# Kernel tuning notes

Measured on AMD Instinct MI355X. Metric: run time of the kernel, lower is better.

## Reference

```python
import jax, jax.numpy as jnp
import numpy as np

B, S, H, TOK = 64, 512, 768, 8   # batch rows, tokens/row, hidden, tokens per sentence
K = (B * S) // TOK               # 4096 sentence segments
NUM_CLASSES = 4


def setup_inputs() -> dict:
    key = jax.random.key(0)
    k0, k1, k2, k3 = jax.random.split(key, 4)
    out = jax.random.normal(k0, (B, S, H), dtype=jnp.float32)
    # each row i holds sentences i*64 .. i*64+63, 8 contiguous tokens each
    sent_ids = (jnp.arange(B * S, dtype=jnp.int64) // TOK).reshape(B, S)
    labels = jax.random.randint(k1, (B, S), 0, NUM_CLASSES, dtype=jnp.int64)
    W1 = jax.random.normal(k2, (2 * H, 512), dtype=jnp.float32) * 0.02
    b1 = jnp.zeros((512,), dtype=jnp.float32)
    W2 = jax.random.normal(k3, (512, NUM_CLASSES), dtype=jnp.float32) * 0.02
    b2 = jnp.zeros((NUM_CLASSES,), dtype=jnp.float32)
    return {"out": out, "W1": W1, "b1": b1, "W2": W2, "b2": b2,
            "labels": labels, "sent_ids": sent_ids}


def _ner_forward(out, W1, b1, W2, b2, labels, sent_ids):
    ids = sent_ids.reshape(-1)                      # [B*S]
    x = out.reshape(-1, H)                          # [B*S, H]
    n = ids.shape[0]
    valid = ids >= 0                                # -1 means padding
    seg = jnp.where(valid, ids, K).astype(jnp.int32)  # route invalid to dummy slot K
    w = valid.astype(out.dtype)

    # masked segment mean of token embeddings (avg_vector)
    counts = jax.ops.segment_sum(w, seg, num_segments=K + 1)[:K]            # [K]
    sums = jax.ops.segment_sum(x * w[:, None], seg, num_segments=K + 1)[:K]  # [K,H]
    seg_mean = sums / jnp.maximum(counts, 1.0)[:, None]

    # build_dict: cls vector of segment k = out[i][0] of LAST row containing k
    row = jnp.arange(n) // S
    cls_row = jax.ops.segment_max(jnp.where(valid, row, -1), seg, num_segments=K + 1)[:K]
    cls_vec = out[jnp.maximum(cls_row, 0), 0]       # [K, H]

    # segment label = labels[mask][0] (first token in flattened order)
    first_idx = jax.ops.segment_min(jnp.where(valid, jnp.arange(n), n), seg,
                                    num_segments=K + 1)[:K]
    seg_label = labels.reshape(-1)[jnp.minimum(first_idx, n - 1)]  # [K]

    feats = jnp.concatenate([cls_vec, seg_mean], axis=1)  # [K, 2H]
    h = jax.nn.relu(feats @ W1 + b1)                      # dropout is identity in eval
    probs = jax.nn.softmax(h @ W2 + b2, axis=1)           # [K, 4]

    # Multiclass_Focal_Loss: gather prob at label, -log, sorted truncated sum
    p = jnp.take_along_axis(probs, seg_label[:, None].astype(jnp.int32), axis=1)[:, 0]
    costs = -jnp.log(p)                                   # [K]
    pos = seg_label > 0
    Npos = jnp.sum(pos)
    neg_costs = jnp.where(seg_label == 0, costs, -jnp.inf)
    sorted_desc = -jnp.sort(-neg_costs)                   # descending
    M = jnp.floor(2.5 * Npos.astype(jnp.float32)).astype(jnp.int32)
    take = (jnp.arange(K) < M) & jnp.isfinite(sorted_desc)
    total = jnp.sum(jnp.where(pos, costs, 0.0)) + jnp.sum(jnp.where(take, sorted_desc, 0.0))
    denom = jnp.floor(3.5 * Npos.astype(jnp.float32))
    return total / denom


def reference(out, W1, b1, W2, b2, labels, sent_ids):
    return _ner_forward(out, W1, b1, W2, b2, labels, sent_ids)
```

## Files before the change

### kernel.cpp

```cpp
#include <hip/hip_runtime.h>
#include <hip/hip_bf16.h>
#include <math.h>

#define SDIM 512
#define HDIM 768
#define TOKN 8
#define KSEG 4096
#define HID 512
#define NCLS 4
#define NPANEL 16

typedef __attribute__((ext_vector_type(8))) short short8v;
typedef __attribute__((ext_vector_type(4))) float f32x4;

__device__ __forceinline__ ushort f2bf(float f) {
    union { float f; unsigned u; } x; x.f = f;
    return (ushort)((x.u + 0x7FFFu + ((x.u >> 16) & 1u)) >> 16);
}

__global__ __launch_bounds__(256) void fused_prep_k(const float* __restrict__ outp,
                                                    const float* __restrict__ W1,
                                                    ushort* __restrict__ segm,
                                                    ushort* __restrict__ W1t,
                                                    float* __restrict__ clsW,
                                                    float* __restrict__ gaccf,
                                                    unsigned* __restrict__ gcnt) {
    __shared__ __align__(16) char smem[18432];
    int bid = blockIdx.x, tid = threadIdx.x;

    if (bid < 8) {
        ushort (*As)[72] = (ushort(*)[72])smem;
        ushort (*Bs)[72] = (ushort(*)[72])(smem + 9216);
        if (bid == 0) {
            if (tid < 2) gaccf[tid] = 0.f;
            if (tid < 3) gcnt[tid] = 0u;
        }
        int nc = bid * 64;
        int lane = tid & 63, wid = tid >> 6;
        int wm = wid >> 1, wn = wid & 1;
        f32x4 acc[2][2] = {};
        int am = tid >> 2, aq = tid & 3;
        int bk = tid >> 4, bq = tid & 15;
        for (int kt = 0; kt < HDIM; kt += 64) {
#pragma unroll
            for (int i = 0; i < 4; ++i) {
                int k = aq * 16 + i * 4;
                float4 v = *(const float4*)(outp + (size_t)am * SDIM * HDIM + kt + k);
                ushort4 u;
                u.x = f2bf(v.x); u.y = f2bf(v.y); u.z = f2bf(v.z); u.w = f2bf(v.w);
                *(ushort4*)(&As[am][k]) = u;
            }
#pragma unroll
            for (int i = 0; i < 4; ++i) {
                int krow = bk + i * 16;
                int n4 = bq * 4;
                float4 v = *(const float4*)(W1 + (size_t)(kt + krow) * HID + nc + n4);
                Bs[n4 + 0][krow] = f2bf(v.x);
                Bs[n4 + 1][krow] = f2bf(v.y);
                Bs[n4 + 2][krow] = f2bf(v.z);
                Bs[n4 + 3][krow] = f2bf(v.w);
            }
            __syncthreads();
            int row = lane & 15, kc = lane >> 4;
#pragma unroll
            for (int ks = 0; ks < 2; ++ks) {
                int kk = ks * 32 + kc * 8;
                short8v afrag[2], bfrag[2];
#pragma unroll
                for (int f = 0; f < 2; ++f) {
                    afrag[f] = *(const short8v*)(&As[wm * 32 + f * 16 + row][kk]);
                    bfrag[f] = *(const short8v*)(&Bs[wn * 32 + f * 16 + row][kk]);
                }
#pragma unroll
                for (int mf = 0; mf < 2; ++mf)
#pragma unroll
                    for (int nf = 0; nf < 2; ++nf)
                        acc[mf][nf] = __builtin_amdgcn_mfma_f32_16x16x32_bf16(
                            afrag[mf], bfrag[nf], acc[mf][nf], 0, 0, 0);
            }
            __syncthreads();
        }
        int col = lane & 15, rg = lane >> 4;
#pragma unroll
        for (int mf = 0; mf < 2; ++mf)
#pragma unroll
            for (int nf = 0; nf < 2; ++nf) {
                int gn = nc + wn * 32 + nf * 16 + col;
#pragma unroll
                for (int r = 0; r < 4; ++r) {
                    int gm = wm * 32 + mf * 16 + rg * 4 + r;
                    clsW[gm * HID + gn] = acc[mf][nf][r];
                }
            }
    } else if (bid < 8 + 384) {
        float (*tile)[33] = (float(*)[33])smem;
        int idx = bid - 8;
        int k0 = (idx % 24) * 32;
        int n0 = (idx / 24) * 32;
        int tx = tid & 31, ty = tid >> 5;
#pragma unroll
        for (int i = 0; i < 4; ++i) {
            int kl = ty + i * 8;
            tile[kl][tx] = W1[(size_t)(HDIM + k0 + kl) * HID + n0 + tx];
        }
        __syncthreads();
#pragma unroll
        for (int i = 0; i < 4; ++i) {
            int nl = ty + i * 8;
            W1t[(size_t)(n0 + nl) * HDIM + k0 + tx] = f2bf(tile[tx][nl]);
        }
    } else {
        int s0 = (bid - 392) * 4;
#pragma unroll
        for (int i = 0; i < 3; ++i) {
            int o = tid + i * 256;
            int s4 = o / 192;
            int c  = o % 192;
            const float4* base = (const float4*)outp +
                                 (size_t)(s0 + s4) * (TOKN * HDIM / 4) + c;
            float x = 0.f, y = 0.f, z = 0.f, w = 0.f;
#pragma unroll
            for (int t = 0; t < TOKN; ++t) {
                float4 v = base[t * (HDIM / 4)];
                x += v.x; y += v.y; z += v.z; w += v.w;
            }
            ushort4 m;
            m.x = f2bf(x * 0.125f); m.y = f2bf(y * 0.125f);
            m.z = f2bf(z * 0.125f); m.w = f2bf(w * 0.125f);
            ((ushort4*)(segm + (size_t)(s0 + s4) * HDIM))[c] = m;
        }
    }
}

#define BM 64
#define BN 64
#define BKK 64

__global__ __launch_bounds__(256) void gemm_head_k(const ushort* __restrict__ A,
                                                   const ushort* __restrict__ Bt,
                                                   const float* __restrict__ clsW,
                                                   const float* __restrict__ b1,
                                                   const float* __restrict__ W2,
                                                   float* __restrict__ plog) {
    __shared__ ushort As[BM][72];
    __shared__ ushort Bs[BN][72];

    int tid = threadIdx.x, lane = tid & 63, wid = tid >> 6;
    int wm = wid >> 1, wn = wid & 1;
    int m0 = blockIdx.x * BM, n0 = blockIdx.y * BN;
    int r_a = tid >> 3, c_a = tid & 7;

    f32x4 acc[2][2] = {};
    float4 pa[2], pb[2];

#pragma unroll
    for (int i = 0; i < 2; ++i) {
        pa[i] = *(const float4*)(A  + (size_t)(m0 + r_a + 32 * i) * HDIM + c_a * 8);
        pb[i] = *(const float4*)(Bt + (size_t)(n0 + r_a + 32 * i) * HDIM + c_a * 8);
    }

    for (int kt = 0; kt < HDIM; kt += BKK) {
#pragma unroll
        for (int i = 0; i < 2; ++i) {
            *(float4*)(&As[r_a + 32 * i][c_a * 8]) = pa[i];
            *(float4*)(&Bs[r_a + 32 * i][c_a * 8]) = pb[i];
        }
        __syncthreads();
        int nkt = kt + BKK;
        if (nkt < HDIM) {
#pragma unroll
            for (int i = 0; i < 2; ++i) {
                pa[i] = *(const float4*)(A  + (size_t)(m0 + r_a + 32 * i) * HDIM + nkt + c_a * 8);
                pb[i] = *(const float4*)(Bt + (size_t)(n0 + r_a + 32 * i) * HDIM + nkt + c_a * 8);
            }
        }
        int row = lane & 15, kc = lane >> 4;
#pragma unroll
        for (int ks = 0; ks < 2; ++ks) {
            int kk = ks * 32 + kc * 8;
            short8v afrag[2], bfrag[2];
#pragma unroll
            for (int f = 0; f < 2; ++f) {
                afrag[f] = *(const short8v*)(&As[wm * 32 + f * 16 + row][kk]);
                bfrag[f] = *(const short8v*)(&Bs[wn * 32 + f * 16 + row][kk]);
            }
#pragma unroll
            for (int mf = 0; mf < 2; ++mf)
#pragma unroll
                for (int nf = 0; nf < 2; ++nf)
                    acc[mf][nf] = __builtin_amdgcn_mfma_f32_16x16x32_bf16(
                        afrag[mf], bfrag[nf], acc[mf][nf], 0, 0, 0);
        }
        __syncthreads();
    }

    int col = lane & 15, rg = lane >> 4;
    float4 w2v[2];
#pragma unroll
    for (int nf = 0; nf < 2; ++nf) {
        int gn = n0 + wn * 32 + nf * 16 + col;
        float bb = b1[gn];
        float cw = clsW[blockIdx.x * HID + gn];
        w2v[nf] = *(const float4*)(W2 + gn * 4);
#pragma unroll
        for (int mf = 0; mf < 2; ++mf)
#pragma unroll
            for (int r = 0; r < 4; ++r)
                acc[mf][nf][r] = fmaxf(acc[mf][nf][r] + cw + bb, 0.f);
    }
    int panel = blockIdx.y * 2 + wn;
#pragma unroll
    for (int c = 0; c < NCLS; ++c) {
        float w0 = (c == 0) ? w2v[0].x : (c == 1) ? w2v[0].y : (c == 2) ? w2v[0].z : w2v[0].w;
        float w1 = (c == 0) ? w2v[1].x : (c == 1) ? w2v[1].y : (c == 2) ? w2v[1].z : w2v[1].w;
        float p[2][4];
#pragma unroll
        for (int mf = 0; mf < 2; ++mf)
#pragma unroll
            for (int r = 0; r < 4; ++r)
                p[mf][r] = fmaf(acc[mf][0][r], w0, acc[mf][1][r] * w1);
#pragma unroll
        for (int off = 1; off < 16; off <<= 1)
#pragma unroll
            for (int mf = 0; mf < 2; ++mf)
#pragma unroll
                for (int r = 0; r < 4; ++r)
                    p[mf][r] += __shfl_xor(p[mf][r], off);
        if (col == 0) {
#pragma unroll
            for (int mf = 0; mf < 2; ++mf)
#pragma unroll
                for (int r = 0; r < 4; ++r) {
                    int gm = m0 + wm * 32 + mf * 16 + rg * 4 + r;
                    plog[((size_t)panel * KSEG + gm) * NCLS + c] = p[mf][r];
                }
        }
    }
}

__global__ __launch_bounds__(256) void loss_k(const float* __restrict__ plog,
                                              const float* __restrict__ b2,
                                              const int* __restrict__ labels,
                                              float* __restrict__ gaccf,
                                              unsigned* __restrict__ gcnt,
                                              float* __restrict__ negs,
                                              float* __restrict__ res) {
    __shared__ float s_p[4], s_n[4];
    __shared__ unsigned s_pc[4], s_nc[4];
    __shared__ int s_last;
    int tid = threadIdx.x, bid = blockIdx.x;
    int lane = tid & 63, wid = tid >> 6;
    float b20 = b2[0], b21 = b2[1], b22 = b2[2], b23 = b2[3];

    float psum = 0.f, nsum = 0.f;
    unsigned pcnt = 0, ncnt = 0;
#pragma unroll
    for (int i = 0; i < 2; ++i) {
        int k = bid * 512 + i * 256 + tid;
        float l0 = b20, l1 = b21, l2 = b22, l3 = b23;
#pragma unroll
        for (int pn = 0; pn < NPANEL; ++pn) {
            float4 v = *(const float4*)(plog + ((size_t)pn * KSEG + k) * NCLS);
            l0 += v.x; l1 += v.y; l2 += v.z; l3 += v.w;
        }
        int lb = labels[k * TOKN];
        float mx = fmaxf(fmaxf(l0, l1), fmaxf(l2, l3));
        float se = expf(l0 - mx) + expf(l1 - mx) + expf(l2 - mx) + expf(l3 - mx);
        float ll = (lb == 0) ? l0 : (lb == 1) ? l1 : (lb == 2) ? l2 : l3;
        float ck = logf(se) + mx - ll;
        if (lb > 0) { psum += ck; pcnt++; } else { nsum += ck; ncnt++; }
    }
#pragma unroll
    for (int off = 32; off; off >>= 1) {
        psum += __shfl_down(psum, off);
        nsum += __shfl_down(nsum, off);
        pcnt += __shfl_down(pcnt, off);
        ncnt += __shfl_down(ncnt, off);
    }
    if (lane == 0) { s_p[wid] = psum; s_n[wid] = nsum; s_pc[wid] = pcnt; s_nc[wid] = ncnt; }
    __syncthreads();
    if (tid == 0) {
        float bp = s_p[0] + s_p[1] + s_p[2] + s_p[3];
        float bn = s_n[0] + s_n[1] + s_n[2] + s_n[3];
        unsigned bpc = s_pc[0] + s_pc[1] + s_pc[2] + s_pc[3];
        unsigned bnc = s_nc[0] + s_nc[1] + s_nc[2] + s_nc[3];
        atomicAdd(&gaccf[0], bp);
        atomicAdd(&gaccf[1], bn);
        atomicAdd(&gcnt[0], bpc);
        atomicAdd(&gcnt[1], bnc);
    }
    __threadfence();
    if (tid == 0) {
        unsigned t = atomicAdd(&gcnt[2], 1u);
        s_last = (t == 7) ? 1 : 0;
    }
    __syncthreads();
    if (!s_last) return;
    __threadfence();

    float tp = __hip_atomic_load(&gaccf[0], __ATOMIC_RELAXED, __HIP_MEMORY_SCOPE_AGENT);
    float tn = __hip_atomic_load(&gaccf[1], __ATOMIC_RELAXED, __HIP_MEMORY_SCOPE_AGENT);
    unsigned np = __hip_atomic_load(&gcnt[0], __ATOMIC_RELAXED, __HIP_MEMORY_SCOPE_AGENT);
    unsigned nn = __hip_atomic_load(&gcnt[1], __ATOMIC_RELAXED, __HIP_MEMORY_SCOPE_AGENT);
    int M = (int)floorf(2.5f * (float)np);
    if ((int)nn <= M) {
        if (tid == 0) res[0] = (tp + tn) / floorf(3.5f * (float)np);
        return;
    }

    for (int k = tid; k < KSEG; k += 256) {
        float l0 = b20, l1 = b21, l2 = b22, l3 = b23;
        for (int pn = 0; pn < NPANEL; ++pn) {
            float4 v = *(const float4*)(plog + ((size_t)pn * KSEG + k) * NCLS);
            l0 += v.x; l1 += v.y; l2 += v.z; l3 += v.w;
        }
        int lb = labels[k * TOKN];
        float mx = fmaxf(fmaxf(l0, l1), fmaxf(l2, l3));
        float se = expf(l0 - mx) + expf(l1 - mx) + expf(l2 - mx) + expf(l3 - mx);
        float ll = (lb == 0) ? l0 : (lb == 1) ? l1 : (lb == 2) ? l2 : l3;
        float ck = logf(se) + mx - ll;
        negs[k] = (lb == 0) ? ck : -INFINITY;
    }
    __syncthreads();
    for (int kk = 2; kk <= KSEG; kk <<= 1) {
        for (int j = kk >> 1; j > 0; j >>= 1) {
            for (int i = tid; i < KSEG; i += 256) {
                int ixj = i ^ j;
                if (ixj > i) {
                    float a = negs[i], b = negs[ixj];
                    bool up = ((i & kk) == 0);
                    if (up ? (a > b) : (a < b)) { negs[i] = b; negs[ixj] = a; }
                }
            }
            __syncthreads();
        }
    }
    float s = 0.f;
    for (int i = tid; i < M; i += 256) {
        float v = negs[KSEG - 1 - i];
        if (isfinite(v)) s += v;
    }
#pragma unroll
    for (int off = 32; off; off >>= 1) s += __shfl_down(s, off);
    if (lane == 0) s_p[wid] = s;
    __syncthreads();
    if (tid == 0) {
        float t = s_p[0] + s_p[1] + s_p[2] + s_p[3];
        res[0] = (tp + t) / floorf(3.5f * (float)np);
    }
}

extern "C" void kernel_launch(void* const* d_in, const int* in_sizes, int n_in,
                              void* d_out, int out_size, void* d_ws, size_t ws_size,
                              hipStream_t stream) {
    const float* outp   = (const float*)d_in[0];
    const float* W1     = (const float*)d_in[1];
    const float* b1     = (const float*)d_in[2];
    const float* W2     = (const float*)d_in[3];
    const float* b2     = (const float*)d_in[4];
    const int*   labels = (const int*)d_in[5];

    char* ws = (char*)d_ws;
    ushort*   segm  = (ushort*)ws;
    ushort*   W1t   = (ushort*)(ws + 6291456);
    float*    clsW  = (float*) (ws + 7077888);
    float*    plog  = (float*) (ws + 7208960);
    float*    negs  = (float*) (ws + 8257536);
    float*    gaccf = (float*) (ws + 8273920);
    unsigned* gcnt  = (unsigned*)(ws + 8273928);
    float*    res   = (float*)d_out;

    fused_prep_k<<<8 + 384 + 1024, 256, 0, stream>>>(outp, W1, segm, W1t, clsW,
                                                     gaccf, gcnt);
    gemm_head_k<<<dim3(KSEG / BM, HID / BN), 256, 0, stream>>>(
        segm, W1t, clsW, b1, W2, plog);
    loss_k<<<8, 256, 0, stream>>>(plog, b2, labels, gaccf, gcnt, negs, res);
}
```

Before: 70.83 us.

## Split segment-mean into own kernel, store fp32 and convert to bf16 in GEMM

The segment-mean work moves out of the fused prep kernel into a dedicated kernel with one block per segment, and the means are stored as fp32 instead of bf16. The GEMM now loads fp32 A tiles and converts them to bf16 while writing shared memory, and the small prep work runs as its own launch. The aim is a simpler, better-balanced seg-mean pass, at the cost of an extra kernel launch and twice the bytes for the intermediate (written once, read by the GEMM). The loss kernel also recomputes M locally before the truncated sum.

```diff
diff --git a/kernel.cpp b/kernel.cpp
--- a/kernel.cpp
+++ b/kernel.cpp
@@ -18,9 +18,23 @@
     return (ushort)((x.u + 0x7FFFu + ((x.u >> 16) & 1u)) >> 16);
 }
 
-__global__ __launch_bounds__(256) void fused_prep_k(const float* __restrict__ outp,
+__global__ __launch_bounds__(192) void seg_mean_k(const float* __restrict__ outp,
+                                                  float* __restrict__ segm) {
+    int k = blockIdx.x;
+    int c = threadIdx.x;
+    const float4* base = (const float4*)(outp + (size_t)k * TOKN * HDIM) + c;
+    float x = 0.f, y = 0.f, z = 0.f, w = 0.f;
+#pragma unroll
+    for (int t = 0; t < TOKN; ++t) {
+        float4 v = base[t * (HDIM / 4)];
+        x += v.x; y += v.y; z += v.z; w += v.w;
+    }
+    float4 m = make_float4(x * 0.125f, y * 0.125f, z * 0.125f, w * 0.125f);
+    ((float4*)(segm + (size_t)k * HDIM))[c] = m;
+}
+
+__global__ __launch_bounds__(256) void prep_small_k(const float* __restrict__ outp,
                                                     const float* __restrict__ W1,
-                                                    ushort* __restrict__ segm,
                                                     ushort* __restrict__ W1t,
                                                     float* __restrict__ clsW,
                                                     float* __restrict__ gaccf,
@@ -92,7 +106,7 @@
                     clsW[gm * HID + gn] = acc[mf][nf][r];
                 }
             }
-    } else if (bid < 8 + 384) {
+    } else {
         float (*tile)[33] = (float(*)[33])smem;
         int idx = bid - 8;
         int k0 = (idx % 24) * 32;
@@ -109,26 +123,6 @@
             int nl = ty + i * 8;
             W1t[(size_t)(n0 + nl) * HDIM + k0 + tx] = f2bf(tile[tx][nl]);
         }
-    } else {
-        int s0 = (bid - 392) * 4;
-#pragma unroll
-        for (int i = 0; i < 3; ++i) {
-            int o = tid + i * 256;
-            int s4 = o / 192;
-            int c  = o % 192;
-            const float4* base = (const float4*)outp +
-                                 (size_t)(s0 + s4) * (TOKN * HDIM / 4) + c;
-            float x = 0.f, y = 0.f, z = 0.f, w = 0.f;
-#pragma unroll
-            for (int t = 0; t < TOKN; ++t) {
-                float4 v = base[t * (HDIM / 4)];
-                x += v.x; y += v.y; z += v.z; w += v.w;
-            }
-            ushort4 m;
-            m.x = f2bf(x * 0.125f); m.y = f2bf(y * 0.125f);
-            m.z = f2bf(z * 0.125f); m.w = f2bf(w * 0.125f);
-            ((ushort4*)(segm + (size_t)(s0 + s4) * HDIM))[c] = m;
-        }
     }
 }
 
@@ -136,7 +130,7 @@
 #define BN 64
 #define BKK 64
 
-__global__ __launch_bounds__(256) void gemm_head_k(const ushort* __restrict__ A,
+__global__ __launch_bounds__(256) void gemm_head_k(const float* __restrict__ A,
                                                    const ushort* __restrict__ Bt,
                                                    const float* __restrict__ clsW,
                                                    const float* __restrict__ b1,
@@ -148,31 +142,39 @@
     int tid = threadIdx.x, lane = tid & 63, wid = tid >> 6;
     int wm = wid >> 1, wn = wid & 1;
     int m0 = blockIdx.x * BM, n0 = blockIdx.y * BN;
-    int r_a = tid >> 3, c_a = tid & 7;
+    int ar = tid >> 2, ac = tid & 3;
+    int br = tid >> 3, bc = tid & 7;
 
     f32x4 acc[2][2] = {};
-    float4 pa[2], pb[2];
-
-#pragma unroll
-    for (int i = 0; i < 2; ++i) {
-        pa[i] = *(const float4*)(A  + (size_t)(m0 + r_a + 32 * i) * HDIM + c_a * 8);
-        pb[i] = *(const float4*)(Bt + (size_t)(n0 + r_a + 32 * i) * HDIM + c_a * 8);
-    }
+    float4 pa[4], pb[2];
+
+#pragma unroll
+    for (int i = 0; i < 4; ++i)
+        pa[i] = *(const float4*)(A + (size_t)(m0 + ar) * HDIM + ac * 16 + i * 4);
+#pragma unroll
+    for (int i = 0; i < 2; ++i)
+        pb[i] = *(const float4*)(Bt + (size_t)(n0 + br + 32 * i) * HDIM + bc * 8);
 
     for (int kt = 0; kt < HDIM; kt += BKK) {
 #pragma unroll
-        for (int i = 0; i < 2; ++i) {
-            *(float4*)(&As[r_a + 32 * i][c_a * 8]) = pa[i];
-            *(float4*)(&Bs[r_a + 32 * i][c_a * 8]) = pb[i];
-        }
+        for (int i = 0; i < 4; ++i) {
+            ushort4 u;
+            u.x = f2bf(pa[i].x); u.y = f2bf(pa[i].y);
+            u.z = f2bf(pa[i].z); u.w = f2bf(pa[i].w);
+            *(ushort4*)(&As[ar][ac * 16 + i * 4]) = u;
+        }
+#pragma unroll
+        for (int i = 0; i < 2; ++i)
+            *(float4*)(&Bs[br + 32 * i][bc * 8]) = pb[i];
         __syncthreads();
         int nkt = kt + BKK;
         if (nkt < HDIM) {
 #pragma unroll
-            for (int i = 0; i < 2; ++i) {
-                pa[i] = *(const float4*)(A  + (size_t)(m0 + r_a + 32 * i) * HDIM + nkt + c_a * 8);
-                pb[i] = *(const float4*)(Bt + (size_t)(n0 + r_a + 32 * i) * HDIM + nkt + c_a * 8);
-            }
+            for (int i = 0; i < 4; ++i)
+                pa[i] = *(const float4*)(A + (size_t)(m0 + ar) * HDIM + nkt + ac * 16 + i * 4);
+#pragma unroll
+            for (int i = 0; i < 2; ++i)
+                pb[i] = *(const float4*)(Bt + (size_t)(n0 + br + 32 * i) * HDIM + nkt + bc * 8);
         }
         int row = lane & 15, kc = lane >> 4;
 #pragma unroll
@@ -335,8 +337,9 @@
             __syncthreads();
         }
     }
+    int M2 = (int)floorf(2.5f * (float)np);
     float s = 0.f;
-    for (int i = tid; i < M; i += 256) {
+    for (int i = tid; i < M2; i += 256) {
         float v = negs[KSEG - 1 - i];
         if (isfinite(v)) s += v;
     }
@@ -361,17 +364,17 @@
     const int*   labels = (const int*)d_in[5];
 
     char* ws = (char*)d_ws;
-    ushort*   segm  = (ushort*)ws;
-    ushort*   W1t   = (ushort*)(ws + 6291456);
-    float*    clsW  = (float*) (ws + 7077888);
-    float*    plog  = (float*) (ws + 7208960);
-    float*    negs  = (float*) (ws + 8257536);
-    float*    gaccf = (float*) (ws + 8273920);
-    unsigned* gcnt  = (unsigned*)(ws + 8273928);
+    float*    segm  = (float*) ws;
+    ushort*   W1t   = (ushort*)(ws + 12582912);
+    float*    clsW  = (float*) (ws + 13369344);
+    float*    plog  = (float*) (ws + 13500416);
+    float*    negs  = (float*) (ws + 14548992);
+    float*    gaccf = (float*) (ws + 14565376);
+    unsigned* gcnt  = (unsigned*)(ws + 14565384);
     float*    res   = (float*)d_out;
 
-    fused_prep_k<<<8 + 384 + 1024, 256, 0, stream>>>(outp, W1, segm, W1t, clsW,
-                                                     gaccf, gcnt);
+    seg_mean_k<<<KSEG, 192, 0, stream>>>(outp, segm);
+    prep_small_k<<<392, 256, 0, stream>>>(outp, W1, W1t, clsW, gaccf, gcnt);
     gemm_head_k<<<dim3(KSEG / BM, HID / BN), 256, 0, stream>>>(
         segm, W1t, clsW, b1, W2, plog);
     loss_k<<<8, 256, 0, stream>>>(plog, b2, labels, gaccf, gcnt, negs, res);
```

Result: faster. 68.94 us (-2.7%).
